# Performance work log

Hardware: AMD Instinct MI355X
Metric: run time of the kernel (lower is better)

## Reference

```python
import jax, jax.numpy as jnp
import numpy as np

V, E, H = 348, 512, 1024  # vocab, embed dim, GRU hidden


def gru_cell(x, h, w_ih, w_hh, b_ih, b_hh):
    # PyTorch GRUCell: gates ordered [r, z, n] along the 3H axis
    gi = x @ w_ih.T + b_ih            # [B, 3H]
    gh = h @ w_hh.T + b_hh            # [B, 3H]
    i_r, i_z, i_n = jnp.split(gi, 3, axis=-1)
    h_r, h_z, h_n = jnp.split(gh, 3, axis=-1)
    r = jax.nn.sigmoid(i_r + h_r)
    z = jax.nn.sigmoid(i_z + h_z)
    n = jnp.tanh(i_n + r * h_n)
    return (1.0 - z) * n + z * h


def setup_inputs() -> dict:
    key = jax.random.key(0)
    ks = jax.random.split(key, 20)
    B, T = 256, 128
    p = lambda k, shape: jax.random.normal(k, shape, dtype=jnp.float32) * 0.02
    return {
        "target": jax.random.randint(ks[0], (B, T), 0, V, dtype=jnp.int32),
        "bos": 1,
        "emb": p(ks[1], (V, E)),
        "w_ih1": p(ks[2], (3 * H, E)),  "w_hh1": p(ks[3], (3 * H, H)),
        "b_ih1": p(ks[4], (3 * H,)),    "b_hh1": p(ks[5], (3 * H,)),
        "w_ih2": p(ks[6], (3 * H, H)),  "w_hh2": p(ks[7], (3 * H, H)),
        "b_ih2": p(ks[8], (3 * H,)),    "b_hh2": p(ks[9], (3 * H,)),
        "w_ih3": p(ks[10], (3 * H, H)), "w_hh3": p(ks[11], (3 * H, H)),
        "b_ih3": p(ks[12], (3 * H,)),   "b_hh3": p(ks[13], (3 * H,)),
        "w_out": p(ks[14], (V, H)),     "b_out": p(ks[15], (V,)),
    }


def reference(target, bos, emb, w_ih1, w_hh1, b_ih1, b_hh1,
              w_ih2, w_hh2, b_ih2, b_hh2,
              w_ih3, w_hh3, b_ih3, b_hh3, w_out, b_out):
    B, T = target.shape
    # input tokens = [<bos>, target[:, :-1]]
    x_in = jnp.concatenate(
        [jnp.full((B, 1), bos, dtype=target.dtype), target[:, :-1]], axis=1)
    h0 = jnp.zeros((B, H), jnp.float32)
    lp0 = jnp.zeros((B,), jnp.float32)

    def step(carry, xt):
        h1, h2, h3, lp = carry
        tok, tgt = xt                     # [B], [B]
        e = emb[tok]                      # [B, E]
        h1 = gru_cell(e, h1, w_ih1, w_hh1, b_ih1, b_hh1)
        h2 = gru_cell(h1, h2, w_ih2, w_hh2, b_ih2, b_hh2)
        h3 = gru_cell(h2, h3, w_ih3, w_hh3, b_ih3, b_hh3)
        logits = h3 @ w_out.T + b_out     # [B, V]
        logp = jax.nn.log_softmax(logits, axis=-1)
        # NLLLoss in source = sum(one_hot(tgt) * log_prob) = gathered log-prob
        lp = lp + jnp.take_along_axis(logp, tgt[:, None], axis=1)[:, 0]
        return (h1, h2, h3, lp), None

    (_, _, _, log_probs), _ = jax.lax.scan(
        step, (h0, h0, h0, lp0), (x_in.T, target.T))
    return log_probs
```

## Files before the change

kernel.cpp:

```cpp
#include <hip/hip_runtime.h>
#include <hip/hip_bf16.h>
#include <cstdint>

constexpr int kT = 128;
constexpr int kB = 256;
constexpr int kE = 512;
constexpr int kH = 1024;
constexpr int kV = 348;
constexpr int kNG = 3072;
constexpr int NB = 208;

constexpr float kScale = 32.f;
constexpr float kInvSS = 1.f / 1024.f;

typedef float f4v __attribute__((ext_vector_type(4)));
typedef unsigned short u16;
typedef unsigned char u8;

__device__ __forceinline__ u8 f2e4m3(float x) {
  int p = __builtin_amdgcn_cvt_pk_fp8_f32(x, x, 0, false);
  return (u8)(p & 0xff);
}

__device__ __forceinline__ uint64_t ldv_u64(const void* p) {
  return __hip_atomic_load((const uint64_t*)p, __ATOMIC_RELAXED, __HIP_MEMORY_SCOPE_AGENT);
}
__device__ __forceinline__ void stv_u8(u8* p, u8 v) {
  __hip_atomic_store(p, v, __ATOMIC_RELAXED, __HIP_MEMORY_SCOPE_AGENT);
}

__device__ __forceinline__ int permn(int n) {
  int gate = n >> 10, j = n & 1023;
  return ((j >> 4) * 48) + gate * 16 + (j & 15);
}

struct Params {
  const int* target; const int* bosp; const float* b_out;
  const u8 *w1i, *w1h, *w2i, *w2h, *w3i, *w3h, *wout, *embb;
  const float *bi1, *bh1, *bi2, *bh2, *bi3, *bh3;
  float *h1f, *h2f, *h3f;
  u8    *h1b, *h2b, *h3b;
  float *lp;
  unsigned *acnt; unsigned *gflag;
};

union SMem {
  struct { u8 A[128 * 144]; u8 B[96 * 144]; } mm;
  float logits[16 * 400];
};

__device__ __forceinline__ void gbar(unsigned* acnt, unsigned* gflag, unsigned s) {
  asm volatile("s_waitcnt vmcnt(0)" ::: "memory");
  __syncthreads();
  if (threadIdx.x == 0) {
    const unsigned g = blockIdx.x & 31u;
    __hip_atomic_fetch_add(&acnt[g * 16], 1u, __ATOMIC_RELAXED, __HIP_MEMORY_SCOPE_AGENT);
    if (blockIdx.x == 0) {
      for (;;) {
        unsigned sum = 0;
#pragma unroll
        for (int i = 0; i < 32; ++i)
          sum += __hip_atomic_load(&acnt[i * 16], __ATOMIC_RELAXED, __HIP_MEMORY_SCOPE_AGENT);
        if (sum >= (unsigned)NB * (s + 1u)) break;
        __builtin_amdgcn_s_sleep(4);
      }
#pragma unroll
      for (int i = 0; i < 32; ++i)
        __hip_atomic_store(&gflag[i * 16], s + 1u, __ATOMIC_RELAXED, __HIP_MEMORY_SCOPE_AGENT);
    } else {
      while (__hip_atomic_load(&gflag[g * 16], __ATOMIC_RELAXED, __HIP_MEMORY_SCOPE_AGENT) <= s)
        __builtin_amdgcn_s_sleep(8);
    }
    asm volatile("" ::: "memory");
  }
  __syncthreads();
}

template<int K, bool EMB>
__device__ __forceinline__ void mm_phase(SMem& sm, const u8* __restrict__ Asrc,
    const u8* __restrict__ W, int b0, int n0,
    f4v* aR, f4v* aZ, f4v* aN,
    const int* __restrict__ target, int bos, int u)
{
  const int t = threadIdx.x, lane = t & 63, wv = t >> 6;
  const int wm = wv >> 1, wg = wv & 1, li = lane & 15, q = lane >> 4;
  uint64_t ra[4][2];
  uint4 rb[3];

  auto stage = [&](int k0) {
#pragma unroll
    for (int p = 0; p < 4; ++p) {
      int id = p * 256 + t, r = id >> 3, c = id & 7;
      if (EMB) {
        int tok = (u == 0) ? bos : target[(b0 + r) * kT + (u - 1)];
        uint4 v = *(const uint4*)&Asrc[(size_t)tok * K + k0 + c * 16];
        ra[p][0] = ((uint64_t)v.y << 32) | v.x;
        ra[p][1] = ((uint64_t)v.w << 32) | v.z;
      } else {
        const u8* src = Asrc + (size_t)(b0 + r) * kH + k0 + c * 16;
        ra[p][0] = ldv_u64(src); ra[p][1] = ldv_u64(src + 8);
      }
    }
#pragma unroll
    for (int p = 0; p < 3; ++p) {
      int id = p * 256 + t, r = id >> 3, c = id & 7;
      rb[p] = *(const uint4*)&W[(size_t)(n0 + r) * K + k0 + c * 16];
    }
  };

  stage(0);
  for (int it = 0; it < K / 128; ++it) {
    __syncthreads();
#pragma unroll
    for (int p = 0; p < 4; ++p) {
      int id = p * 256 + t, r = id >> 3, c = id & 7;
      *(uint64_t*)&sm.mm.A[r * 144 + c * 16] = ra[p][0];
      *(uint64_t*)&sm.mm.A[r * 144 + c * 16 + 8] = ra[p][1];
    }
#pragma unroll
    for (int p = 0; p < 3; ++p) {
      int id = p * 256 + t, r = id >> 3, c = id & 7;
      *(uint4*)&sm.mm.B[r * 144 + c * 16] = rb[p];
    }
    __syncthreads();
    if (it + 1 < K / 128) stage((it + 1) * 128);
#pragma unroll
    for (int kk = 0; kk < 128; kk += 32) {
      int lk = kk + q * 8;
      long a[4], bb[3];
#pragma unroll
      for (int m2 = 0; m2 < 4; ++m2)
        a[m2] = *(const long*)&sm.mm.A[(64 * wm + 16 * m2 + li) * 144 + lk];
#pragma unroll
      for (int g = 0; g < 3; ++g)
        bb[g] = *(const long*)&sm.mm.B[(48 * wg + 16 * g + li) * 144 + lk];
#pragma unroll
      for (int m2 = 0; m2 < 4; ++m2) {
        aR[m2] = __builtin_amdgcn_mfma_f32_16x16x32_fp8_fp8(a[m2], bb[0], aR[m2], 0, 0, 0);
        aZ[m2] = __builtin_amdgcn_mfma_f32_16x16x32_fp8_fp8(a[m2], bb[1], aZ[m2], 0, 0, 0);
        aN[m2] = __builtin_amdgcn_mfma_f32_16x16x32_fp8_fp8(a[m2], bb[2], aN[m2], 0, 0, 0);
      }
    }
  }
}

template<int K1, bool L1>
__device__ void do_L(SMem& sm, const u8* __restrict__ xsrc,
                     const u8* __restrict__ hbPrev, const float* __restrict__ hfPrev,
                     const u8* __restrict__ Wih, const u8* __restrict__ Whh,
                     const float* __restrict__ biP, const float* __restrict__ bhP,
                     float* __restrict__ hfOut, u8* __restrict__ hbOut,
                     const int* __restrict__ target, int bos, int u, int mt, int jt)
{
  const int b0 = mt * 128, j0 = jt * 32, n0 = jt * 96;
  f4v aR[4], aZ[4], aNi[4], aNh[4];
#pragma unroll
  for (int i = 0; i < 4; ++i) {
    aR[i] = f4v{0.f,0.f,0.f,0.f}; aZ[i] = f4v{0.f,0.f,0.f,0.f};
    aNi[i] = f4v{0.f,0.f,0.f,0.f}; aNh[i] = f4v{0.f,0.f,0.f,0.f};
  }
  mm_phase<K1, L1>(sm, xsrc, Wih, b0, n0, aR, aZ, aNi, target, bos, u);
  mm_phase<kH, false>(sm, hbPrev, Whh, b0, n0, aR, aZ, aNh, target, bos, u);

  const int t = threadIdx.x, lane = t & 63, wv = t >> 6;
  const int wm = wv >> 1, wg = wv & 1, li = lane & 15, q = lane >> 4;
  const int j = j0 + 16 * wg + li;
  const int cr = n0 + 48 * wg + li;
  const float bR = biP[cr] + bhP[cr];
  const float bZ = biP[cr + 16] + bhP[cr + 16];
  const float biN = biP[cr + 32], bhN = bhP[cr + 32];
  float hold[4][4];
#pragma unroll
  for (int m2 = 0; m2 < 4; ++m2)
#pragma unroll
    for (int r = 0; r < 4; ++r) {
      int b = b0 + 64 * wm + 16 * m2 + 4 * q + r;
      hold[m2][r] = hfPrev[(size_t)b * kH + j];
    }
#pragma unroll
  for (int m2 = 0; m2 < 4; ++m2)
#pragma unroll
    for (int r = 0; r < 4; ++r) {
      int b = b0 + 64 * wm + 16 * m2 + 4 * q + r;
      float rg = 1.f / (1.f + __expf(-(aR[m2][r] * kInvSS + bR)));
      float zg = 1.f / (1.f + __expf(-(aZ[m2][r] * kInvSS + bZ)));
      float np = (aNi[m2][r] * kInvSS + biN) + rg * (aNh[m2][r] * kInvSS + bhN);
      float nh = 2.f / (1.f + __expf(-2.f * np)) - 1.f;
      float hnew = (1.f - zg) * nh + zg * hold[m2][r];
      hfOut[(size_t)b * kH + j] = hnew;
      stv_u8(&hbOut[(size_t)b * kH + j], f2e4m3(hnew * kScale));
    }
}

__device__ void do_E(SMem& sm, const u8* __restrict__ h3b, const u8* __restrict__ wo,
                     const float* __restrict__ b_out, const int* __restrict__ target,
                     float* __restrict__ lp, int u, int tile)
{
  const int b0 = tile * 16;
  const int t = threadIdx.x, lane = t & 63, wv = t >> 6;
  const int li = lane & 15, q = lane >> 4;
  f4v acc[6];
#pragma unroll
  for (int f = 0; f < 6; ++f) acc[f] = f4v{0.f, 0.f, 0.f, 0.f};

  const u8* ap = h3b + (size_t)(b0 + li) * kH + q * 8;
  uint64_t aCur = ldv_u64(ap);
  uint64_t bCur[6], bNx[6];
#pragma unroll
  for (int f = 0; f < 6; ++f)
    bCur[f] = *(const uint64_t*)&wo[(size_t)(96 * wv + 16 * f + li) * kH + q * 8];
  for (int k0 = 0; k0 < kH; k0 += 32) {
    uint64_t aNx = 0;
    if (k0 + 32 < kH) {
      aNx = ldv_u64(ap + k0 + 32);
#pragma unroll
      for (int f = 0; f < 6; ++f)
        bNx[f] = *(const uint64_t*)&wo[(size_t)(96 * wv + 16 * f + li) * kH + k0 + 32 + q * 8];
    }
#pragma unroll
    for (int f = 0; f < 6; ++f)
      acc[f] = __builtin_amdgcn_mfma_f32_16x16x32_fp8_fp8((long)aCur, (long)bCur[f], acc[f], 0, 0, 0);
    aCur = aNx;
#pragma unroll
    for (int f = 0; f < 6; ++f) bCur[f] = bNx[f];
  }
#pragma unroll
  for (int f = 0; f < 6; ++f) {
    int n = 96 * wv + 16 * f + li;
    if (n < kV) {
      float bo = b_out[n];
#pragma unroll
      for (int r = 0; r < 4; ++r)
        sm.logits[(4 * q + r) * 400 + n] = acc[f][r] * kInvSS + bo;
    }
  }
  __syncthreads();
  int m = 4 * wv + q;
  int b = b0 + m;
  float mx = -1e30f;
  for (int cc = li; cc < kV; cc += 16) mx = fmaxf(mx, sm.logits[m * 400 + cc]);
#pragma unroll
  for (int d = 1; d < 16; d <<= 1) mx = fmaxf(mx, __shfl_xor(mx, d, 16));
  float se = 0.f;
  for (int cc = li; cc < kV; cc += 16) se += __expf(sm.logits[m * 400 + cc] - mx);
#pragma unroll
  for (int d = 1; d < 16; d <<= 1) se += __shfl_xor(se, d, 16);
  int tgt = target[b * kT + u];
  float logp = sm.logits[m * 400 + tgt] - mx - __logf(se);
  if (li == 0) lp[b] += logp;
}

__global__ __launch_bounds__(256, 1) void rnn_main(Params P)
{
  __shared__ SMem sm;
  const int bid = blockIdx.x;
  const int bos = P.bosp[0];
  const size_t HS = (size_t)kB * kH;

  const int local = bid & 63;
  const int mt = (local >> 3) & 1;
  const int jt = (local & 7) | ((local >> 4) << 3);

  for (int s = 0; s < kT + 3; ++s) {
    if (bid < 64) {
      int u = s;
      if (u < kT)
        do_L<kE, true>(sm, P.embb,
                       P.h1b + (size_t)((u - 1) & 1) * HS, P.h1f + (size_t)((u - 1) & 1) * HS,
                       P.w1i, P.w1h, P.bi1, P.bh1,
                       P.h1f + (size_t)(u & 1) * HS, P.h1b + (size_t)(u & 1) * HS,
                       P.target, bos, u, mt, jt);
    } else if (bid < 128) {
      int u = s - 1;
      if (u >= 0 && u < kT)
        do_L<kH, false>(sm, P.h1b + (size_t)(u & 1) * HS,
                        P.h2b + (size_t)((u - 1) & 1) * HS, P.h2f + (size_t)((u - 1) & 1) * HS,
                        P.w2i, P.w2h, P.bi2, P.bh2,
                        P.h2f + (size_t)(u & 1) * HS, P.h2b + (size_t)(u & 1) * HS,
                        P.target, bos, u, mt, jt);
    } else if (bid < 192) {
      int u = s - 2;
      if (u >= 0 && u < kT)
        do_L<kH, false>(sm, P.h2b + (size_t)(u & 1) * HS,
                        P.h3b + (size_t)((u - 1) & 1) * HS, P.h3f + (size_t)((u - 1) & 1) * HS,
                        P.w3i, P.w3h, P.bi3, P.bh3,
                        P.h3f + (size_t)(u & 1) * HS, P.h3b + (size_t)(u & 1) * HS,
                        P.target, bos, u, mt, jt);
    } else {
      int u = s - 3;
      if (u >= 0 && u < kT)
        do_E(sm, P.h3b + (size_t)(u & 1) * HS, P.wout, P.b_out, P.target, P.lp, u, bid - 192);
    }
    gbar(P.acnt, P.gflag, (unsigned)s);
  }
}

__global__ void k_conv_w(const float* __restrict__ w, u8* __restrict__ wp, int K, int logK) {
  int idx = blockIdx.x * 256 + threadIdx.x;
  if (idx >= kNG * K) return;
  int n = idx >> logK, k = idx & (K - 1);
  wp[(size_t)permn(n) * K + k] = f2e4m3(w[idx] * kScale);
}
__global__ void k_conv_b(const float* __restrict__ b, float* __restrict__ bp) {
  int idx = blockIdx.x * 256 + threadIdx.x;
  if (idx < kNG) bp[permn(idx)] = b[idx];
}
__global__ void k_conv_wout(const float* __restrict__ w, u8* __restrict__ wp) {
  int idx = blockIdx.x * 256 + threadIdx.x;
  if (idx >= 384 * kH) return;
  int n = idx >> 10, k = idx & 1023;
  wp[idx] = (n < kV) ? f2e4m3(w[(size_t)n * kH + k] * kScale) : (u8)0;
}
__global__ void k_conv_emb(const float* __restrict__ e, u8* __restrict__ ep) {
  int idx = blockIdx.x * 256 + threadIdx.x;
  if (idx < kV * kE) ep[idx] = f2e4m3(e[idx] * kScale);
}

extern "C" void kernel_launch(void* const* d_in, const int* in_sizes, int n_in,
                              void* d_out, int out_size, void* d_ws, size_t ws_size,
                              hipStream_t stream)
{
  const int*   target = (const int*)d_in[0];
  const int*   bosp   = (const int*)d_in[1];
  const float* emb    = (const float*)d_in[2];
  const float* w_ih1  = (const float*)d_in[3];
  const float* w_hh1  = (const float*)d_in[4];
  const float* b_ih1  = (const float*)d_in[5];
  const float* b_hh1  = (const float*)d_in[6];
  const float* w_ih2  = (const float*)d_in[7];
  const float* w_hh2  = (const float*)d_in[8];
  const float* b_ih2  = (const float*)d_in[9];
  const float* b_hh2  = (const float*)d_in[10];
  const float* w_ih3  = (const float*)d_in[11];
  const float* w_hh3  = (const float*)d_in[12];
  const float* b_ih3  = (const float*)d_in[13];
  const float* b_hh3  = (const float*)d_in[14];
  const float* w_out  = (const float*)d_in[15];
  const float* b_out  = (const float*)d_in[16];

  char* ws = (char*)d_ws;
  size_t off = 0;
  auto alloc = [&](size_t bytes) -> void* {
    void* p = ws + off;
    off = (off + bytes + 511) & ~(size_t)511;
    return p;
  };
  u8* w1i = (u8*)alloc((size_t)kNG * kE);
  u8* w1h = (u8*)alloc((size_t)kNG * kH);
  u8* w2i = (u8*)alloc((size_t)kNG * kH);
  u8* w2h = (u8*)alloc((size_t)kNG * kH);
  u8* w3i = (u8*)alloc((size_t)kNG * kH);
  u8* w3h = (u8*)alloc((size_t)kNG * kH);
  u8* wo  = (u8*)alloc((size_t)384 * kH);
  u8* eb  = (u8*)alloc((size_t)kV * kE);
  float* bi1 = (float*)alloc(kNG * 4);
  float* bh1 = (float*)alloc(kNG * 4);
  float* bi2 = (float*)alloc(kNG * 4);
  float* bh2 = (float*)alloc(kNG * 4);
  float* bi3 = (float*)alloc(kNG * 4);
  float* bh3 = (float*)alloc(kNG * 4);
  float* h1f = (float*)alloc((size_t)2 * kB * kH * 4);
  float* h2f = (float*)alloc((size_t)2 * kB * kH * 4);
  float* h3f = (float*)alloc((size_t)2 * kB * kH * 4);
  u8* h1b = (u8*)alloc((size_t)2 * kB * kH);
  u8* h2b = (u8*)alloc((size_t)2 * kB * kH);
  u8* h3b = (u8*)alloc((size_t)2 * kB * kH);
  unsigned* bar = (unsigned*)alloc(4096);
  (void)ws_size; (void)in_sizes; (void)n_in; (void)out_size;

  k_conv_w<<<(kNG * kE + 255) / 256, 256, 0, stream>>>(w_ih1, w1i, kE, 9);
  k_conv_w<<<(kNG * kH + 255) / 256, 256, 0, stream>>>(w_hh1, w1h, kH, 10);
  k_conv_w<<<(kNG * kH + 255) / 256, 256, 0, stream>>>(w_ih2, w2i, kH, 10);
  k_conv_w<<<(kNG * kH + 255) / 256, 256, 0, stream>>>(w_hh2, w2h, kH, 10);
  k_conv_w<<<(kNG * kH + 255) / 256, 256, 0, stream>>>(w_ih3, w3i, kH, 10);
  k_conv_w<<<(kNG * kH + 255) / 256, 256, 0, stream>>>(w_hh3, w3h, kH, 10);
  k_conv_b<<<(kNG + 255) / 256, 256, 0, stream>>>(b_ih1, bi1);
  k_conv_b<<<(kNG + 255) / 256, 256, 0, stream>>>(b_hh1, bh1);
  k_conv_b<<<(kNG + 255) / 256, 256, 0, stream>>>(b_ih2, bi2);
  k_conv_b<<<(kNG + 255) / 256, 256, 0, stream>>>(b_hh2, bh2);
  k_conv_b<<<(kNG + 255) / 256, 256, 0, stream>>>(b_ih3, bi3);
  k_conv_b<<<(kNG + 255) / 256, 256, 0, stream>>>(b_hh3, bh3);
  k_conv_wout<<<(384 * kH + 255) / 256, 256, 0, stream>>>(w_out, wo);
  k_conv_emb<<<(kV * kE + 255) / 256, 256, 0, stream>>>(emb, eb);

  hipMemsetAsync(h1f, 0, (size_t)3 * 2 * kB * kH * 4, stream);
  hipMemsetAsync(h1b, 0, (size_t)3 * 2 * kB * kH, stream);
  hipMemsetAsync(bar, 0, 4096, stream);
  hipMemsetAsync(d_out, 0, (size_t)kB * 4, stream);

  Params P;
  P.target = target; P.bosp = bosp; P.b_out = b_out;
  P.w1i = w1i; P.w1h = w1h; P.w2i = w2i; P.w2h = w2h; P.w3i = w3i; P.w3h = w3h;
  P.wout = wo; P.embb = eb;
  P.bi1 = bi1; P.bh1 = bh1; P.bi2 = bi2; P.bh2 = bh2; P.bi3 = bi3; P.bh3 = bh3;
  P.h1f = h1f; P.h2f = h2f; P.h3f = h3f;
  P.h1b = h1b; P.h2b = h2b; P.h3b = h3b;
  P.lp = (float*)d_out;
  P.acnt = bar; P.gflag = bar + 512;

  rnn_main<<<dim3(NB), dim3(256), 0, stream>>>(P);
}
```

Measured before the change: 4.532 ms.

## Store per-timestep fp8 hidden states, use plain vector loads, double-buffer register staging

The fp8 hidden-state buffers now hold every timestep instead of a two-slot ping-pong. Because each address is written only once, the relaxed atomic 64-bit loads can become ordinary 128-bit vector loads. The staging registers are double-buffered so global loads run two K-tiles ahead of the MFMA work, and at step zero the recurrent input is zero-filled instead of read from a memset buffer. The cost is a much larger workspace and more registers. Plain loads may also be served stale from non-coherent caches across workgroups, since correctness now depends on never-written addresses being fetched fresh.

```diff
diff --git a/kernel.cpp b/kernel.cpp
--- a/kernel.cpp
+++ b/kernel.cpp
@@ -22,9 +22,6 @@
   return (u8)(p & 0xff);
 }
 
-__device__ __forceinline__ uint64_t ldv_u64(const void* p) {
-  return __hip_atomic_load((const uint64_t*)p, __ATOMIC_RELAXED, __HIP_MEMORY_SCOPE_AGENT);
-}
 __device__ __forceinline__ void stv_u8(u8* p, u8 v) {
   __hip_atomic_store(p, v, __ATOMIC_RELAXED, __HIP_MEMORY_SCOPE_AGENT);
 }
@@ -77,53 +74,53 @@
 }
 
 template<int K, bool EMB>
-__device__ __forceinline__ void mm_phase(SMem& sm, const u8* __restrict__ Asrc,
+__device__ __forceinline__ void mm_phase(SMem& sm, const u8* __restrict__ Asrc, bool zeroA,
     const u8* __restrict__ W, int b0, int n0,
     f4v* aR, f4v* aZ, f4v* aN,
     const int* __restrict__ target, int bos, int u)
 {
   const int t = threadIdx.x, lane = t & 63, wv = t >> 6;
   const int wm = wv >> 1, wg = wv & 1, li = lane & 15, q = lane >> 4;
-  uint64_t ra[4][2];
-  uint4 rb[3];
-
-  auto stage = [&](int k0) {
+  constexpr int nIt = K / 128;
+  uint4 ra[2][4];
+  uint4 rb[2][3];
+
+  auto stage = [&](int d, int k0) {
 #pragma unroll
     for (int p = 0; p < 4; ++p) {
       int id = p * 256 + t, r = id >> 3, c = id & 7;
       if (EMB) {
         int tok = (u == 0) ? bos : target[(b0 + r) * kT + (u - 1)];
-        uint4 v = *(const uint4*)&Asrc[(size_t)tok * K + k0 + c * 16];
-        ra[p][0] = ((uint64_t)v.y << 32) | v.x;
-        ra[p][1] = ((uint64_t)v.w << 32) | v.z;
+        ra[d][p] = *(const uint4*)&Asrc[(size_t)tok * K + k0 + c * 16];
+      } else if (zeroA) {
+        ra[d][p] = uint4{0u, 0u, 0u, 0u};
       } else {
-        const u8* src = Asrc + (size_t)(b0 + r) * kH + k0 + c * 16;
-        ra[p][0] = ldv_u64(src); ra[p][1] = ldv_u64(src + 8);
+        ra[d][p] = *(const uint4*)&Asrc[(size_t)(b0 + r) * K + k0 + c * 16];
       }
     }
 #pragma unroll
     for (int p = 0; p < 3; ++p) {
       int id = p * 256 + t, r = id >> 3, c = id & 7;
-      rb[p] = *(const uint4*)&W[(size_t)(n0 + r) * K + k0 + c * 16];
+      rb[d][p] = *(const uint4*)&W[(size_t)(n0 + r) * K + k0 + c * 16];
     }
   };
 
-  stage(0);
-  for (int it = 0; it < K / 128; ++it) {
+  stage(0, 0);
+  if (nIt > 1) stage(1, 128);
+  for (int it = 0; it < nIt; ++it) {
     __syncthreads();
 #pragma unroll
     for (int p = 0; p < 4; ++p) {
       int id = p * 256 + t, r = id >> 3, c = id & 7;
-      *(uint64_t*)&sm.mm.A[r * 144 + c * 16] = ra[p][0];
-      *(uint64_t*)&sm.mm.A[r * 144 + c * 16 + 8] = ra[p][1];
+      *(uint4*)&sm.mm.A[r * 144 + c * 16] = ra[it & 1][p];
     }
 #pragma unroll
     for (int p = 0; p < 3; ++p) {
       int id = p * 256 + t, r = id >> 3, c = id & 7;
-      *(uint4*)&sm.mm.B[r * 144 + c * 16] = rb[p];
+      *(uint4*)&sm.mm.B[r * 144 + c * 16] = rb[it & 1][p];
     }
     __syncthreads();
-    if (it + 1 < K / 128) stage((it + 1) * 128);
+    if (it + 2 < nIt) stage(it & 1, (it + 2) * 128);
 #pragma unroll
     for (int kk = 0; kk < 128; kk += 32) {
       int lk = kk + q * 8;
@@ -146,7 +143,8 @@
 
 template<int K1, bool L1>
 __device__ void do_L(SMem& sm, const u8* __restrict__ xsrc,
-                     const u8* __restrict__ hbPrev, const float* __restrict__ hfPrev,
+                     const u8* __restrict__ hbPrev, bool zeroH,
+                     const float* __restrict__ hfPrev,
                      const u8* __restrict__ Wih, const u8* __restrict__ Whh,
                      const float* __restrict__ biP, const float* __restrict__ bhP,
                      float* __restrict__ hfOut, u8* __restrict__ hbOut,
@@ -159,8 +157,8 @@
     aR[i] = f4v{0.f,0.f,0.f,0.f}; aZ[i] = f4v{0.f,0.f,0.f,0.f};
     aNi[i] = f4v{0.f,0.f,0.f,0.f}; aNh[i] = f4v{0.f,0.f,0.f,0.f};
   }
-  mm_phase<K1, L1>(sm, xsrc, Wih, b0, n0, aR, aZ, aNi, target, bos, u);
-  mm_phase<kH, false>(sm, hbPrev, Whh, b0, n0, aR, aZ, aNh, target, bos, u);
+  mm_phase<K1, L1>(sm, xsrc, false, Wih, b0, n0, aR, aZ, aNi, target, bos, u);
+  mm_phase<kH, false>(sm, hbPrev, zeroH, Whh, b0, n0, aR, aZ, aNh, target, bos, u);
 
   const int t = threadIdx.x, lane = t & 63, wv = t >> 6;
   const int wm = wv >> 1, wg = wv & 1, li = lane & 15, q = lane >> 4;
@@ -192,7 +190,7 @@
     }
 }
 
-__device__ void do_E(SMem& sm, const u8* __restrict__ h3b, const u8* __restrict__ wo,
+__device__ void do_E(SMem& sm, const u8* __restrict__ h3u, const u8* __restrict__ wo,
                      const float* __restrict__ b_out, const int* __restrict__ target,
                      float* __restrict__ lp, int u, int tile)
 {
@@ -203,8 +201,8 @@
 #pragma unroll
   for (int f = 0; f < 6; ++f) acc[f] = f4v{0.f, 0.f, 0.f, 0.f};
 
-  const u8* ap = h3b + (size_t)(b0 + li) * kH + q * 8;
-  uint64_t aCur = ldv_u64(ap);
+  const u8* ap = h3u + (size_t)(b0 + li) * kH + q * 8;
+  uint64_t aCur = *(const uint64_t*)ap;
   uint64_t bCur[6], bNx[6];
 #pragma unroll
   for (int f = 0; f < 6; ++f)
@@ -212,7 +210,7 @@
   for (int k0 = 0; k0 < kH; k0 += 32) {
     uint64_t aNx = 0;
     if (k0 + 32 < kH) {
-      aNx = ldv_u64(ap + k0 + 32);
+      aNx = *(const uint64_t*)(ap + k0 + 32);
 #pragma unroll
       for (int f = 0; f < 6; ++f)
         bNx[f] = *(const uint64_t*)&wo[(size_t)(96 * wv + 16 * f + li) * kH + k0 + 32 + q * 8];
@@ -224,6 +222,7 @@
 #pragma unroll
     for (int f = 0; f < 6; ++f) bCur[f] = bNx[f];
   }
+  __syncthreads();
 #pragma unroll
   for (int f = 0; f < 6; ++f) {
     int n = 96 * wv + 16 * f + li;
@@ -266,30 +265,33 @@
       int u = s;
       if (u < kT)
         do_L<kE, true>(sm, P.embb,
-                       P.h1b + (size_t)((u - 1) & 1) * HS, P.h1f + (size_t)((u - 1) & 1) * HS,
+                       P.h1b + (size_t)(u > 0 ? u - 1 : 0) * HS, u == 0,
+                       P.h1f + (size_t)((u - 1) & 1) * HS,
                        P.w1i, P.w1h, P.bi1, P.bh1,
-                       P.h1f + (size_t)(u & 1) * HS, P.h1b + (size_t)(u & 1) * HS,
+                       P.h1f + (size_t)(u & 1) * HS, P.h1b + (size_t)u * HS,
                        P.target, bos, u, mt, jt);
     } else if (bid < 128) {
       int u = s - 1;
       if (u >= 0 && u < kT)
-        do_L<kH, false>(sm, P.h1b + (size_t)(u & 1) * HS,
-                        P.h2b + (size_t)((u - 1) & 1) * HS, P.h2f + (size_t)((u - 1) & 1) * HS,
+        do_L<kH, false>(sm, P.h1b + (size_t)u * HS,
+                        P.h2b + (size_t)(u > 0 ? u - 1 : 0) * HS, u == 0,
+                        P.h2f + (size_t)((u - 1) & 1) * HS,
                         P.w2i, P.w2h, P.bi2, P.bh2,
-                        P.h2f + (size_t)(u & 1) * HS, P.h2b + (size_t)(u & 1) * HS,
+                        P.h2f + (size_t)(u & 1) * HS, P.h2b + (size_t)u * HS,
                         P.target, bos, u, mt, jt);
     } else if (bid < 192) {
       int u = s - 2;
       if (u >= 0 && u < kT)
-        do_L<kH, false>(sm, P.h2b + (size_t)(u & 1) * HS,
-                        P.h3b + (size_t)((u - 1) & 1) * HS, P.h3f + (size_t)((u - 1) & 1) * HS,
+        do_L<kH, false>(sm, P.h2b + (size_t)u * HS,
+                        P.h3b + (size_t)(u > 0 ? u - 1 : 0) * HS, u == 0,
+                        P.h3f + (size_t)((u - 1) & 1) * HS,
                         P.w3i, P.w3h, P.bi3, P.bh3,
-                        P.h3f + (size_t)(u & 1) * HS, P.h3b + (size_t)(u & 1) * HS,
+                        P.h3f + (size_t)(u & 1) * HS, P.h3b + (size_t)u * HS,
                         P.target, bos, u, mt, jt);
     } else {
       int u = s - 3;
       if (u >= 0 && u < kT)
-        do_E(sm, P.h3b + (size_t)(u & 1) * HS, P.wout, P.b_out, P.target, P.lp, u, bid - 192);
+        do_E(sm, P.h3b + (size_t)u * HS, P.wout, P.b_out, P.target, P.lp, u, bid - 192);
     }
     gbar(P.acnt, P.gflag, (unsigned)s);
   }
@@ -362,10 +364,10 @@
   float* h1f = (float*)alloc((size_t)2 * kB * kH * 4);
   float* h2f = (float*)alloc((size_t)2 * kB * kH * 4);
   float* h3f = (float*)alloc((size_t)2 * kB * kH * 4);
-  u8* h1b = (u8*)alloc((size_t)2 * kB * kH);
-  u8* h2b = (u8*)alloc((size_t)2 * kB * kH);
-  u8* h3b = (u8*)alloc((size_t)2 * kB * kH);
-  unsigned* bar = (unsigned*)alloc(4096);
+  u8* h1b = (u8*)alloc((size_t)kT * kB * kH);
+  u8* h2b = (u8*)alloc((size_t)kT * kB * kH);
+  u8* h3b = (u8*)alloc((size_t)kT * kB * kH);
+  unsigned* bar = (unsigned*)alloc(8192);
   (void)ws_size; (void)in_sizes; (void)n_in; (void)out_size;
 
   k_conv_w<<<(kNG * kE + 255) / 256, 256, 0, stream>>>(w_ih1, w1i, kE, 9);
@@ -384,8 +386,7 @@
   k_conv_emb<<<(kV * kE + 255) / 256, 256, 0, stream>>>(emb, eb);
 
   hipMemsetAsync(h1f, 0, (size_t)3 * 2 * kB * kH * 4, stream);
-  hipMemsetAsync(h1b, 0, (size_t)3 * 2 * kB * kH, stream);
-  hipMemsetAsync(bar, 0, 4096, stream);
+  hipMemsetAsync(bar, 0, 8192, stream);
   hipMemsetAsync(d_out, 0, (size_t)kB * 4, stream);
 
   Params P;
```

Result: slower. 5.872 ms (+29.6%).
